# Performance work log

Hardware: AMD Instinct MI355X
Metric: run time of the kernel (lower is better)

## Reference

```python
import jax, jax.numpy as jnp
import numpy as np

N_HEADS = 16
B = 8
SEQ = 1024
HID = 1024
TOT = B * SEQ


def setup_inputs() -> dict:
    key = jax.random.key(0)
    k1, k2, k3 = jax.random.split(key, 3)
    hidden_states = jax.random.normal(k1, (TOT, HID), dtype=jnp.float32)
    Wqkv = jax.random.normal(k2, (3 * HID, HID), dtype=jnp.float32) * 0.02
    Bqkv = jax.random.normal(k3, (3 * HID,), dtype=jnp.float32) * 0.02
    cu_seqlens = (jnp.arange(B + 1, dtype=jnp.int32) * SEQ)
    return {"hidden_states": hidden_states, "Wqkv": Wqkv, "Bqkv": Bqkv,
            "cu_seqlens": cu_seqlens, "max_s": SEQ}


def reference(hidden_states, Wqkv, Bqkv, cu_seqlens, max_s):
    # qkv projection: F.linear(hidden, Wqkv, Bqkv) -> [T, 3H]
    T, H = hidden_states.shape
    h = N_HEADS
    d = H // h
    b = cu_seqlens.shape[0] - 1
    S = T // b  # equal-length packing; cu_seqlens = arange(b+1)*S
    qkv = hidden_states @ Wqkv.T + Bqkv                      # [T, 3H]
    qkv = qkv.reshape(b, S, 3, h, d)
    q, k, v = qkv[:, :, 0], qkv[:, :, 1], qkv[:, :, 2]       # [b, S, h, d]
    scale = 1.0 / jnp.sqrt(jnp.asarray(d, dtype=q.dtype))
    scores = jnp.einsum("bshd,bthd->bhst", q, k) * scale     # [b, h, S, S]
    probs = jax.nn.softmax(scores, axis=-1)                  # p_dropout = 0.0
    ctx = jnp.einsum("bhst,bthd->bshd", probs, v)            # [b, S, h, d]
    return ctx.reshape(T, H)
```

## Files before the change

kernel.cpp:

```cpp
#include <hip/hip_runtime.h>

typedef __attribute__((ext_vector_type(8))) __bf16 bf16x8;
typedef __attribute__((ext_vector_type(2))) __bf16 bf16x2;
typedef __attribute__((ext_vector_type(4))) float f32x4;
typedef __attribute__((ext_vector_type(4))) unsigned int u32x4;

#define AS1 __attribute__((address_space(1)))
#define AS3 __attribute__((address_space(3)))

__device__ __forceinline__ unsigned short f2b(float f) {
    union { float f; unsigned int u; } c; c.f = f;
    unsigned int r = c.u + 0x7fffu + ((c.u >> 16) & 1u);
    return (unsigned short)(r >> 16);
}

__device__ __forceinline__ unsigned int pack2(float a, float b) {
    bf16x2 t;
    t[0] = (__bf16)a;
    t[1] = (__bf16)b;
    return __builtin_bit_cast(unsigned int, t);
}

__device__ __forceinline__ void gload_lds16(const void* g, void* l) {
    __builtin_amdgcn_global_load_lds((const AS1 unsigned int*)g,
                                     (AS3 unsigned int*)l, 16, 0, 0);
}

__global__ void cvt2_kernel(const float* __restrict__ in0,
                            unsigned short* __restrict__ out0, int n0,
                            const float* __restrict__ in1,
                            unsigned short* __restrict__ out1, int n1) {
    int i = blockIdx.x * blockDim.x + threadIdx.x;
    int stride = gridDim.x * blockDim.x;
    const int nt = n0 + n1;
    for (; i < nt; i += stride) {
        if (i < n0) {
            float4 v = reinterpret_cast<const float4*>(in0)[i];
            ushort4 o;
            o.x = f2b(v.x); o.y = f2b(v.y); o.z = f2b(v.z); o.w = f2b(v.w);
            reinterpret_cast<ushort4*>(out0)[i] = o;
        } else {
            const int j = i - n0;
            float4 v = reinterpret_cast<const float4*>(in1)[j];
            ushort4 o;
            o.x = f2b(v.x); o.y = f2b(v.y); o.z = f2b(v.z); o.w = f2b(v.w);
            reinterpret_cast<ushort4*>(out1)[j] = o;
        }
    }
}

__global__ __launch_bounds__(512, 2) void qkv_gemm(
    const unsigned short* __restrict__ A,
    const unsigned short* __restrict__ Bw,
    const float* __restrict__ bias,
    unsigned short* __restrict__ qb,
    unsigned short* __restrict__ kb,
    unsigned short* __restrict__ vb)
{
    __shared__ __align__(16) char smem[147456];
    const int tid = threadIdx.x;
    const int lane = tid & 63, w = tid >> 6;
    const int wm = w >> 1, wn = w & 1;
    const int wg = (blockIdx.x & 7) * 96 + (blockIdx.x >> 3);
    const int mt = wg / 24;
    const int nt = wg % 24;
    const int fr = lane & 15, kg = lane >> 4;

    const int sr = lane >> 3;
    const int gl = (lane & 7) ^ sr;
    const unsigned short* a_srcg = A + (size_t)(mt * 256 + w * 8 + sr) * 1024 + gl * 8;
    const unsigned short* b_srcg = Bw + (size_t)(nt * 128 + w * 8 + sr) * 1024 + gl * 8;

    f32x4 acc[4][4] = {};
    const int pgk[2] = { ((0 + kg) ^ (fr & 7)) * 16, ((4 + kg) ^ (fr & 7)) * 16 };
    const int aoffA = (wm * 64 + fr) * 128;
    const int boffB = (wn * 64 + fr) * 128;

#define STAGE_FULL(buf, kt) do {                                    \
    char* Sa_ = smem + (buf) * 49152 + w * 1024;                    \
    const size_t ko_ = (size_t)(kt) * 64;                           \
    gload_lds16(a_srcg + ko_,          Sa_);                        \
    gload_lds16(a_srcg + 65536 + ko_,  Sa_ + 8192);                 \
    gload_lds16(a_srcg + 131072 + ko_, Sa_ + 16384);                \
    gload_lds16(a_srcg + 196608 + ko_, Sa_ + 24576);                \
    gload_lds16(b_srcg + ko_,          Sa_ + 32768);                \
    gload_lds16(b_srcg + 65536 + ko_,  Sa_ + 40960);                \
} while (0)

#define MM(m_, n_) do {                                                        \
    acc[m_][n_] = __builtin_amdgcn_mfma_f32_16x16x32_bf16(                     \
        af[m_][0], bf[n_][0], acc[m_][n_], 0, 0, 0);                           \
    acc[m_][n_] = __builtin_amdgcn_mfma_f32_16x16x32_bf16(                     \
        af[m_][1], bf[n_][1], acc[m_][n_], 0, 0, 0);                           \
} while (0)

#define GT4(CUR, PRE, kt, DOSTAGE, WNSTR) do {                                 \
    const char* Ab_ = smem + (CUR) * 49152;                                    \
    const char* Bb_ = Ab_ + 32768;                                             \
    char* Sa_ = smem + (PRE) * 49152 + w * 1024;                               \
    const size_t ko_ = (size_t)((kt) + 2) * 64;                                \
    bf16x8 af[4][2], bf[4][2];                                                 \
    _Pragma("unroll")                                                          \
    for (int n = 0; n < 2; ++n)                                                \
        _Pragma("unroll")                                                      \
        for (int ks = 0; ks < 2; ++ks)                                         \
            bf[n][ks] = *reinterpret_cast<const bf16x8*>(                      \
                Bb_ + boffB + n * 2048 + pgk[ks]);                             \
    _Pragma("unroll")                                                          \
    for (int m = 0; m < 2; ++m)                                                \
        _Pragma("unroll")                                                      \
        for (int ks = 0; ks < 2; ++ks)                                         \
            af[m][ks] = *reinterpret_cast<const bf16x8*>(                      \
                Ab_ + aoffA + m * 2048 + pgk[ks]);                             \
    if (DOSTAGE) {                                                             \
        gload_lds16(a_srcg + ko_,          Sa_);                               \
        gload_lds16(a_srcg + 65536 + ko_,  Sa_ + 8192);                        \
        gload_lds16(a_srcg + 131072 + ko_, Sa_ + 16384);                       \
    }                                                                          \
    __builtin_amdgcn_s_barrier();                                              \
    asm volatile("s_waitcnt lgkmcnt(0)" ::: "memory");                         \
    __builtin_amdgcn_s_setprio(1);                                             \
    MM(0, 0); MM(0, 1); MM(1, 0); MM(1, 1);                                    \
    __builtin_amdgcn_s_setprio(0);                                             \
    _Pragma("unroll")                                                          \
    for (int n = 2; n < 4; ++n)                                                \
        _Pragma("unroll")                                                      \
        for (int ks = 0; ks < 2; ++ks)                                         \
            bf[n][ks] = *reinterpret_cast<const bf16x8*>(                      \
                Bb_ + boffB + n * 2048 + pgk[ks]);                             \
    if (DOSTAGE) {                                                             \
        gload_lds16(a_srcg + 196608 + ko_, Sa_ + 24576);                       \
        gload_lds16(b_srcg + ko_,          Sa_ + 32768);                       \
        gload_lds16(b_srcg + 65536 + ko_,  Sa_ + 40960);                       \
    }                                                                          \
    __builtin_amdgcn_s_barrier();                                              \
    asm volatile("s_waitcnt lgkmcnt(0)" ::: "memory");                         \
    __builtin_amdgcn_s_setprio(1);                                             \
    MM(0, 2); MM(0, 3); MM(1, 2); MM(1, 3);                                    \
    __builtin_amdgcn_s_setprio(0);                                             \
    _Pragma("unroll")                                                          \
    for (int m = 2; m < 4; ++m)                                                \
        _Pragma("unroll")                                                      \
        for (int ks = 0; ks < 2; ++ks)                                         \
            af[m][ks] = *reinterpret_cast<const bf16x8*>(                      \
                Ab_ + aoffA + m * 2048 + pgk[ks]);                             \
    __builtin_amdgcn_s_barrier();                                              \
    asm volatile("s_waitcnt lgkmcnt(0)" ::: "memory");                         \
    __builtin_amdgcn_s_setprio(1);                                             \
    MM(2, 0); MM(2, 1); MM(3, 0); MM(3, 1);                                    \
    __builtin_amdgcn_s_setprio(0);                                             \
    asm volatile("s_waitcnt vmcnt(" WNSTR ")" ::: "memory");                   \
    __builtin_amdgcn_s_barrier();                                              \
    __builtin_amdgcn_s_setprio(1);                                             \
    MM(2, 2); MM(2, 3); MM(3, 2); MM(3, 3);                                    \
    __builtin_amdgcn_s_setprio(0);                                             \
} while (0)

    STAGE_FULL(0, 0);
    STAGE_FULL(1, 1);
    asm volatile("s_waitcnt vmcnt(6)" ::: "memory");
    __builtin_amdgcn_s_barrier();
#pragma unroll 1
    for (int it = 0; it < 4; ++it) {
        const int t0 = it * 3;
        GT4(0, 2, t0 + 0, 1, "6");
        GT4(1, 0, t0 + 1, 1, "6");
        GT4(2, 1, t0 + 2, 1, "6");
    }
    GT4(0, 2, 12, 1, "6");
    GT4(1, 0, 13, 1, "6");
    GT4(2, 1, 14, 0, "0");
    GT4(0, 0, 15, 0, "0");
    __syncthreads();

    const int sidx = nt >> 3;
    float bv[4];
#pragma unroll
    for (int n = 0; n < 4; ++n) bv[n] = bias[nt * 128 + wn * 64 + n * 16 + fr];

    unsigned short* Cs = (unsigned short*)smem;

    if (sidx < 2) {
        unsigned short* dstb = (sidx == 0) ? qb : kb;
        const float sc = (sidx == 0) ? 0.1803368801111f : 1.0f;
#pragma unroll
        for (int p = 0; p < 2; ++p) {
            if ((wm >> 1) == p) {
                const int r0 = (wm & 1) * 64;
#pragma unroll
                for (int m = 0; m < 4; ++m)
#pragma unroll
                    for (int n = 0; n < 4; ++n)
#pragma unroll
                        for (int r = 0; r < 4; ++r)
                            Cs[(r0 + m * 16 + kg * 4 + r) * 136 + wn * 64 + n * 16 + fr] =
                                f2b((acc[m][n][r] + bv[n]) * sc);
            }
            __syncthreads();
#pragma unroll
            for (int itc = 0; itc < 4; ++itc) {
                const int task = itc * 512 + tid;
                const int rl = task >> 4;
                const int i16 = task & 15;
                const int t = mt * 256 + p * 128 + rl;
                const int b_ = t >> 10, s = t & 1023;
                const int head = ((nt * 128 + i16 * 8) >> 6) & 15;
                u32x4 v = *reinterpret_cast<const u32x4*>(Cs + rl * 136 + i16 * 8);
                *reinterpret_cast<u32x4*>(
                    dstb + ((size_t)(b_ * 16 + head) * 1024 + s) * 64 + (i16 & 7) * 8) = v;
            }
            __syncthreads();
        }
    } else {
#pragma unroll
        for (int p = 0; p < 2; ++p) {
            if ((wm >> 1) == p) {
                const int r0 = (wm & 1) * 64;
#pragma unroll
                for (int m = 0; m < 4; ++m)
#pragma unroll
                    for (int n = 0; n < 4; ++n)
#pragma unroll
                        for (int j = 0; j < 2; ++j) {
                            unsigned int pk = pack2(acc[m][n][2 * j] + bv[n],
                                                    acc[m][n][2 * j + 1] + bv[n]);
                            *reinterpret_cast<unsigned int*>(
                                Cs + (wn * 64 + n * 16 + fr) * 136
                                   + r0 + m * 16 + kg * 4 + 2 * j) = pk;
                        }
            }
            __syncthreads();
#pragma unroll
            for (int itc = 0; itc < 4; ++itc) {
                const int task = itc * 512 + tid;
                const int c = task >> 4;
                const int i16 = task & 15;
                const int col = nt * 128 + c;
                const int head = (col >> 6) & 15;
                const int d = col & 63;
                const int b_ = (mt * 256) >> 10;
                const int s0 = (mt * 256 & 1023) + p * 128 + i16 * 8;
                u32x4 v = *reinterpret_cast<const u32x4*>(Cs + c * 136 + i16 * 8);
                *reinterpret_cast<u32x4*>(
                    vb + (size_t)((b_ * 16 + head) * 64 + d) * 1024 + s0) = v;
            }
            __syncthreads();
        }
    }
#undef STAGE_FULL
#undef GT4
#undef MM
}

#define KVB 64
__global__ __launch_bounds__(256, 4) void attn_kernel(
    const unsigned short* __restrict__ qb,
    const unsigned short* __restrict__ kb,
    const unsigned short* __restrict__ vb,
    float* __restrict__ out)
{
    __shared__ __align__(16) char asmem[32768];
    const int tid = threadIdx.x;
    const int lane = tid & 63, w = tid >> 6;
    const int wg = (blockIdx.x & 7) * 128 + (blockIdx.x >> 3);
    const int bh = wg >> 3;
    const int qt = wg & 7;
    const int b_ = bh >> 4, h_ = bh & 15;
    const int fr = lane & 15, kg = lane >> 4;

    const unsigned short* qp = qb + ((size_t)bh * 1024 + qt * 128) * 64;
    const unsigned short* kp = kb + (size_t)bh * 1024 * 64;
    const unsigned short* vp = vb + (size_t)bh * 64 * 1024;

    bf16x8 qfr[2][2];
#pragma unroll
    for (int qf = 0; qf < 2; ++qf) {
        const unsigned short* qr = qp + (w * 32 + qf * 16 + fr) * 64 + kg * 8;
        qfr[qf][0] = *reinterpret_cast<const bf16x8*>(qr);
        qfr[qf][1] = *reinterpret_cast<const bf16x8*>(qr + 32);
    }

    float m_q[2] = {-1e30f, -1e30f}, l_q[2] = {0.f, 0.f};
    f32x4 o_acc[2][4] = {};

    const int ksr = w * 8 + (lane >> 3);
    const int kcb = (lane & 7) * 16;

#define ASTAGE(buf, kvt) do {                                                  \
    const int kv0_ = (kvt) * KVB;                                              \
    char* Kb_ = asmem + (buf) * 16384 + w * 1024;                              \
    char* Vb_ = Kb_ + 8192;                                                    \
    _Pragma("unroll")                                                          \
    for (int i = 0; i < 2; ++i) {                                              \
        const int st = i * 32 + ksr;                                           \
        const int key = ((st >> 5) << 5) | (((st & 15) >> 2) << 3)             \
                      | (((st >> 4) & 1) << 2) | (st & 3);                     \
        const int scb = kcb ^ ((st & 7) << 4);                                 \
        gload_lds16(kp + (size_t)(kv0_ + key) * 64 + (scb >> 1),               \
                    Kb_ + i * 4096);                                           \
        const int d_ = i * 32 + ksr;                                           \
        const int svb = kcb ^ ((d_ & 7) << 4);                                 \
        gload_lds16(vp + (size_t)d_ * 1024 + kv0_ + (svb >> 1),                \
                    Vb_ + i * 4096);                                           \
    }                                                                          \
} while (0)

#define ACOMP(buf) do {                                                        \
    const char* Kb = asmem + (buf) * 16384;                                    \
    const char* Vb = Kb + 8192;                                                \
    f32x4 sacc[2][4] = {};                                                     \
    __builtin_amdgcn_s_setprio(1);                                             \
    _Pragma("unroll")                                                          \
    for (int jt = 0; jt < 4; ++jt) {                                           \
        _Pragma("unroll")                                                      \
        for (int ks = 0; ks < 2; ++ks) {                                       \
            const int cb = (ks * 64 + kg * 16) ^ ((fr & 7) << 4);              \
            bf16x8 kf = *reinterpret_cast<const bf16x8*>(                      \
                Kb + (jt * 16 + fr) * 128 + cb);                               \
            _Pragma("unroll")                                                  \
            for (int qf = 0; qf < 2; ++qf)                                     \
                sacc[qf][jt] = __builtin_amdgcn_mfma_f32_16x16x32_bf16(        \
                    kf, qfr[qf][ks], sacc[qf][jt], 0, 0, 0);                   \
        }                                                                      \
    }                                                                          \
    __builtin_amdgcn_s_setprio(0);                                             \
    unsigned int P2[2][4][2];                                                  \
    _Pragma("unroll")                                                          \
    for (int qf = 0; qf < 2; ++qf) {                                           \
        float mx = -1e30f;                                                     \
        _Pragma("unroll")                                                      \
        for (int jt = 0; jt < 4; ++jt) {                                       \
            float a = fmaxf(fmaxf(sacc[qf][jt][0], sacc[qf][jt][1]),           \
                            fmaxf(sacc[qf][jt][2], sacc[qf][jt][3]));          \
            mx = fmaxf(mx, a);                                                 \
        }                                                                      \
        mx = fmaxf(mx, __shfl_xor(mx, 16, 64));                                \
        mx = fmaxf(mx, __shfl_xor(mx, 32, 64));                                \
        if (__any(mx > m_q[qf] + 8.0f)) {                                      \
            const float mn = fmaxf(m_q[qf], mx);                               \
            const float corr = __builtin_amdgcn_exp2f(m_q[qf] - mn);           \
            m_q[qf] = mn;                                                      \
            l_q[qf] *= corr;                                                   \
            float cr[4];                                                       \
            _Pragma("unroll")                                                  \
            for (int r = 0; r < 4; ++r)                                        \
                cr[r] = __shfl(corr, kg * 4 + r, 64);                          \
            _Pragma("unroll")                                                  \
            for (int d0 = 0; d0 < 4; ++d0)                                     \
                _Pragma("unroll")                                              \
                for (int r = 0; r < 4; ++r) o_acc[qf][d0][r] *= cr[r];         \
        }                                                                      \
        const float mn_ = m_q[qf];                                             \
        float rs = 0.f;                                                        \
        _Pragma("unroll")                                                      \
        for (int jt = 0; jt < 4; ++jt) {                                       \
            float p0 = __builtin_amdgcn_exp2f(sacc[qf][jt][0] - mn_);          \
            float p1 = __builtin_amdgcn_exp2f(sacc[qf][jt][1] - mn_);          \
            float p2 = __builtin_amdgcn_exp2f(sacc[qf][jt][2] - mn_);          \
            float p3 = __builtin_amdgcn_exp2f(sacc[qf][jt][3] - mn_);          \
            rs += (p0 + p1) + (p2 + p3);                                       \
            P2[qf][jt][0] = pack2(p0, p1);                                     \
            P2[qf][jt][1] = pack2(p2, p3);                                     \
        }                                                                      \
        rs += __shfl_xor(rs, 16, 64);                                          \
        rs += __shfl_xor(rs, 32, 64);                                          \
        l_q[qf] += rs;                                                         \
    }                                                                          \
    __builtin_amdgcn_s_setprio(1);                                             \
    _Pragma("unroll")                                                          \
    for (int c = 0; c < 2; ++c) {                                              \
        bf16x8 pa[2];                                                          \
        _Pragma("unroll")                                                      \
        for (int qf = 0; qf < 2; ++qf) {                                       \
            u32x4 pw = { P2[qf][2 * c][0], P2[qf][2 * c][1],                   \
                         P2[qf][2 * c + 1][0], P2[qf][2 * c + 1][1] };         \
            pa[qf] = __builtin_bit_cast(bf16x8, pw);                           \
        }                                                                      \
        _Pragma("unroll")                                                      \
        for (int d0 = 0; d0 < 4; ++d0) {                                       \
            const int dd = d0 * 16 + fr;                                       \
            const int cbv = (c * 64 + kg * 16) ^ ((dd & 7) << 4);              \
            bf16x8 vf = *reinterpret_cast<const bf16x8*>(Vb + dd * 128 + cbv); \
            _Pragma("unroll")                                                  \
            for (int qf = 0; qf < 2; ++qf)                                     \
                o_acc[qf][d0] = __builtin_amdgcn_mfma_f32_16x16x32_bf16(       \
                    pa[qf], vf, o_acc[qf][d0], 0, 0, 0);                       \
        }                                                                      \
    }                                                                          \
    __builtin_amdgcn_s_setprio(0);                                             \
} while (0)

    ASTAGE(0, 0);
#pragma unroll 1
    for (int t = 0; t < 15; ++t) {
        ASTAGE((t + 1) & 1, t + 1);
        asm volatile("s_waitcnt vmcnt(4) lgkmcnt(0)" ::: "memory");
        __builtin_amdgcn_s_barrier();
        ACOMP(t & 1);
        asm volatile("s_waitcnt lgkmcnt(0)" ::: "memory");
        __builtin_amdgcn_s_barrier();
    }
    asm volatile("s_waitcnt vmcnt(0) lgkmcnt(0)" ::: "memory");
    __builtin_amdgcn_s_barrier();
    ACOMP(1);

#pragma unroll
    for (int qf = 0; qf < 2; ++qf) {
        float linv[4];
#pragma unroll
        for (int r = 0; r < 4; ++r)
            linv[r] = 1.0f / __shfl(l_q[qf], kg * 4 + r, 64);
        const int trow = b_ * 1024 + qt * 128 + w * 32 + qf * 16;
#pragma unroll
        for (int d0 = 0; d0 < 4; ++d0) {
            const int c = h_ * 64 + d0 * 16 + fr;
#pragma unroll
            for (int r = 0; r < 4; ++r)
                out[(size_t)(trow + kg * 4 + r) * 1024 + c] = o_acc[qf][d0][r] * linv[r];
        }
    }
#undef ASTAGE
#undef ACOMP
}

extern "C" void kernel_launch(void* const* d_in, const int* in_sizes, int n_in,
                              void* d_out, int out_size, void* d_ws, size_t ws_size,
                              hipStream_t stream)
{
    const float* hs   = (const float*)d_in[0];
    const float* Wqkv = (const float*)d_in[1];
    const float* Bqkv = (const float*)d_in[2];
    float* out = (float*)d_out;

    char* ws = (char*)d_ws;
    unsigned short* hsb = (unsigned short*)(ws);
    unsigned short* wb  = (unsigned short*)(ws + (size_t)16 * 1048576);
    unsigned short* qb  = (unsigned short*)(ws + (size_t)22 * 1048576);
    unsigned short* kb  = (unsigned short*)(ws + (size_t)38 * 1048576);
    unsigned short* vb  = (unsigned short*)(ws + (size_t)54 * 1048576);

    cvt2_kernel<<<2048, 256, 0, stream>>>(hs, hsb, 8192 * 1024 / 4,
                                          Wqkv, wb, 3072 * 1024 / 4);
    qkv_gemm<<<768, 512, 0, stream>>>(hsb, wb, Bqkv, qb, kb, vb);
    attn_kernel<<<1024, 256, 0, stream>>>(qb, kb, vb, out);
}
```

Baseline: 128.2 us.

## Halve GEMM K-tile to 32 and shared memory to raise occupancy

Shrinks the QKV GEMM K-step from 64 to 32 with a triple-buffered 24KB stage, cutting shared memory from 144KB to 72KB. This allows a higher target occupancy via launch_bounds(512,4). The LDS swizzle and the load mapping are redone for 64-byte rows, and the inner schedule is reduced to two MFMA phases per step. The cost is twice as many K iterations, each with barriers, and less compute per synchronisation. Register pressure may also limit the occupancy actually reached.

Measured after the change: 120.2 us. 1.07x faster.

```diff
diff --git a/kernel.cpp b/kernel.cpp
--- a/kernel.cpp
+++ b/kernel.cpp
@@ -49,7 +49,7 @@
     }
 }
 
-__global__ __launch_bounds__(512, 2) void qkv_gemm(
+__global__ __launch_bounds__(512, 4) void qkv_gemm(
     const unsigned short* __restrict__ A,
     const unsigned short* __restrict__ Bw,
     const float* __restrict__ bias,
@@ -57,7 +57,7 @@
     unsigned short* __restrict__ kb,
     unsigned short* __restrict__ vb)
 {
-    __shared__ __align__(16) char smem[147456];
+    __shared__ __align__(16) char smem[73728];
     const int tid = threadIdx.x;
     const int lane = tid & 63, w = tid >> 6;
     const int wm = w >> 1, wn = w & 1;
@@ -66,111 +66,78 @@
     const int nt = wg % 24;
     const int fr = lane & 15, kg = lane >> 4;
 
-    const int sr = lane >> 3;
-    const int gl = (lane & 7) ^ sr;
-    const unsigned short* a_srcg = A + (size_t)(mt * 256 + w * 8 + sr) * 1024 + gl * 8;
-    const unsigned short* b_srcg = Bw + (size_t)(nt * 128 + w * 8 + sr) * 1024 + gl * 8;
+    const int sr = lane >> 2;
+    const int g  = (lane & 3) ^ ((sr >> 1) & 3);
+    const unsigned short* a_srcg = A  + (size_t)(mt * 256 + w * 16 + sr) * 1024 + g * 8;
+    const unsigned short* b_srcg = Bw + (size_t)(nt * 128 + w * 16 + sr) * 1024 + g * 8;
 
     f32x4 acc[4][4] = {};
-    const int pgk[2] = { ((0 + kg) ^ (fr & 7)) * 16, ((4 + kg) ^ (fr & 7)) * 16 };
-    const int aoffA = (wm * 64 + fr) * 128;
-    const int boffB = (wn * 64 + fr) * 128;
+    const int pg = (kg ^ ((fr >> 1) & 3)) * 16;
+    const int aoffA = (wm * 64 + fr) * 64;
+    const int boffB = (wn * 64 + fr) * 64;
 
 #define STAGE_FULL(buf, kt) do {                                    \
-    char* Sa_ = smem + (buf) * 49152 + w * 1024;                    \
-    const size_t ko_ = (size_t)(kt) * 64;                           \
-    gload_lds16(a_srcg + ko_,          Sa_);                        \
-    gload_lds16(a_srcg + 65536 + ko_,  Sa_ + 8192);                 \
-    gload_lds16(a_srcg + 131072 + ko_, Sa_ + 16384);                \
-    gload_lds16(a_srcg + 196608 + ko_, Sa_ + 24576);                \
-    gload_lds16(b_srcg + ko_,          Sa_ + 32768);                \
-    gload_lds16(b_srcg + 65536 + ko_,  Sa_ + 40960);                \
+    char* Sb_ = smem + (buf) * 24576 + w * 1024;                    \
+    const size_t ko_ = (size_t)(kt) * 32;                           \
+    gload_lds16(a_srcg + ko_,          Sb_);                        \
+    gload_lds16(a_srcg + 131072 + ko_, Sb_ + 8192);                 \
+    gload_lds16(b_srcg + ko_,          Sb_ + 16384);                \
 } while (0)
 
 #define MM(m_, n_) do {                                                        \
     acc[m_][n_] = __builtin_amdgcn_mfma_f32_16x16x32_bf16(                     \
-        af[m_][0], bf[n_][0], acc[m_][n_], 0, 0, 0);                           \
-    acc[m_][n_] = __builtin_amdgcn_mfma_f32_16x16x32_bf16(                     \
-        af[m_][1], bf[n_][1], acc[m_][n_], 0, 0, 0);                           \
+        af[m_], bf[n_], acc[m_][n_], 0, 0, 0);                                 \
 } while (0)
 
-#define GT4(CUR, PRE, kt, DOSTAGE, WNSTR) do {                                 \
-    const char* Ab_ = smem + (CUR) * 49152;                                    \
-    const char* Bb_ = Ab_ + 32768;                                             \
-    char* Sa_ = smem + (PRE) * 49152 + w * 1024;                               \
-    const size_t ko_ = (size_t)((kt) + 2) * 64;                                \
-    bf16x8 af[4][2], bf[4][2];                                                 \
-    _Pragma("unroll")                                                          \
-    for (int n = 0; n < 2; ++n)                                                \
-        _Pragma("unroll")                                                      \
-        for (int ks = 0; ks < 2; ++ks)                                         \
-            bf[n][ks] = *reinterpret_cast<const bf16x8*>(                      \
-                Bb_ + boffB + n * 2048 + pgk[ks]);                             \
+#define GT2(CUR, PRE, kt, DOSTAGE, WNSTR) do {                                 \
+    const char* Ab_ = smem + (CUR) * 24576;                                    \
+    const char* Bb_ = Ab_ + 16384;                                             \
+    char* Sb_ = smem + (PRE) * 24576 + w * 1024;                               \
+    const size_t ko_ = (size_t)((kt) + 2) * 32;                                \
+    bf16x8 af[4], bf[4];                                                       \
+    _Pragma("unroll")                                                          \
+    for (int n = 0; n < 4; ++n)                                                \
+        bf[n] = *reinterpret_cast<const bf16x8*>(Bb_ + boffB + n * 1024 + pg); \
     _Pragma("unroll")                                                          \
     for (int m = 0; m < 2; ++m)                                                \
-        _Pragma("unroll")                                                      \
-        for (int ks = 0; ks < 2; ++ks)                                         \
-            af[m][ks] = *reinterpret_cast<const bf16x8*>(                      \
-                Ab_ + aoffA + m * 2048 + pgk[ks]);                             \
+        af[m] = *reinterpret_cast<const bf16x8*>(Ab_ + aoffA + m * 1024 + pg); \
     if (DOSTAGE) {                                                             \
-        gload_lds16(a_srcg + ko_,          Sa_);                               \
-        gload_lds16(a_srcg + 65536 + ko_,  Sa_ + 8192);                        \
-        gload_lds16(a_srcg + 131072 + ko_, Sa_ + 16384);                       \
+        gload_lds16(a_srcg + ko_,          Sb_);                               \
+        gload_lds16(a_srcg + 131072 + ko_, Sb_ + 8192);                        \
     }                                                                          \
     __builtin_amdgcn_s_barrier();                                              \
     asm volatile("s_waitcnt lgkmcnt(0)" ::: "memory");                         \
     __builtin_amdgcn_s_setprio(1);                                             \
-    MM(0, 0); MM(0, 1); MM(1, 0); MM(1, 1);                                    \
+    MM(0, 0); MM(0, 1); MM(0, 2); MM(0, 3);                                    \
+    MM(1, 0); MM(1, 1); MM(1, 2); MM(1, 3);                                    \
     __builtin_amdgcn_s_setprio(0);                                             \
     _Pragma("unroll")                                                          \
-    for (int n = 2; n < 4; ++n)                                                \
-        _Pragma("unroll")                                                      \
-        for (int ks = 0; ks < 2; ++ks)                                         \
-            bf[n][ks] = *reinterpret_cast<const bf16x8*>(                      \
-                Bb_ + boffB + n * 2048 + pgk[ks]);                             \
+    for (int m = 2; m < 4; ++m)                                                \
+        af[m] = *reinterpret_cast<const bf16x8*>(Ab_ + aoffA + m * 1024 + pg); \
     if (DOSTAGE) {                                                             \
-        gload_lds16(a_srcg + 196608 + ko_, Sa_ + 24576);                       \
-        gload_lds16(b_srcg + ko_,          Sa_ + 32768);                       \
-        gload_lds16(b_srcg + 65536 + ko_,  Sa_ + 40960);                       \
-    }                                                                          \
-    __builtin_amdgcn_s_barrier();                                              \
-    asm volatile("s_waitcnt lgkmcnt(0)" ::: "memory");                         \
-    __builtin_amdgcn_s_setprio(1);                                             \
-    MM(0, 2); MM(0, 3); MM(1, 2); MM(1, 3);                                    \
-    __builtin_amdgcn_s_setprio(0);                                             \
-    _Pragma("unroll")                                                          \
-    for (int m = 2; m < 4; ++m)                                                \
-        _Pragma("unroll")                                                      \
-        for (int ks = 0; ks < 2; ++ks)                                         \
-            af[m][ks] = *reinterpret_cast<const bf16x8*>(                      \
-                Ab_ + aoffA + m * 2048 + pgk[ks]);                             \
-    __builtin_amdgcn_s_barrier();                                              \
-    asm volatile("s_waitcnt lgkmcnt(0)" ::: "memory");                         \
-    __builtin_amdgcn_s_setprio(1);                                             \
-    MM(2, 0); MM(2, 1); MM(3, 0); MM(3, 1);                                    \
-    __builtin_amdgcn_s_setprio(0);                                             \
-    asm volatile("s_waitcnt vmcnt(" WNSTR ")" ::: "memory");                   \
+        gload_lds16(b_srcg + ko_, Sb_ + 16384);                                \
+    }                                                                          \
+    asm volatile("s_waitcnt vmcnt(" WNSTR ") lgkmcnt(0)" ::: "memory");        \
     __builtin_amdgcn_s_barrier();                                              \
     __builtin_amdgcn_s_setprio(1);                                             \
-    MM(2, 2); MM(2, 3); MM(3, 2); MM(3, 3);                                    \
+    MM(2, 0); MM(2, 1); MM(2, 2); MM(2, 3);                                    \
+    MM(3, 0); MM(3, 1); MM(3, 2); MM(3, 3);                                    \
     __builtin_amdgcn_s_setprio(0);                                             \
 } while (0)
 
     STAGE_FULL(0, 0);
     STAGE_FULL(1, 1);
-    asm volatile("s_waitcnt vmcnt(6)" ::: "memory");
+    asm volatile("s_waitcnt vmcnt(3)" ::: "memory");
     __builtin_amdgcn_s_barrier();
 #pragma unroll 1
-    for (int it = 0; it < 4; ++it) {
+    for (int it = 0; it < 10; ++it) {
         const int t0 = it * 3;
-        GT4(0, 2, t0 + 0, 1, "6");
-        GT4(1, 0, t0 + 1, 1, "6");
-        GT4(2, 1, t0 + 2, 1, "6");
-    }
-    GT4(0, 2, 12, 1, "6");
-    GT4(1, 0, 13, 1, "6");
-    GT4(2, 1, 14, 0, "0");
-    GT4(0, 0, 15, 0, "0");
+        GT2(0, 2, t0 + 0, 1, "3");
+        GT2(1, 0, t0 + 1, 1, "3");
+        GT2(2, 1, t0 + 2, 1, "3");
+    }
+    GT2(0, 2, 30, 0, "0");
+    GT2(1, 0, 31, 0, "0");
     __syncthreads();
 
     const int sidx = nt >> 3;
@@ -248,7 +215,7 @@
         }
     }
 #undef STAGE_FULL
-#undef GT4
+#undef GT2
 #undef MM
 }
 
```
